# Kernel optimization log

Hardware: AMD Instinct MI355X
Metric: run time of the kernel (lower is better)

The kernel has to match this reference:

```python
import jax, jax.numpy as jnp
import numpy as np

B, S, D, E, F = 2, 2048, 1024, 8, 4096


def setup_inputs() -> dict:
    key = jax.random.key(0)
    k1, k2, k3, k4 = jax.random.split(key, 4)
    x = jax.random.normal(k1, (B, S, D), dtype=jnp.float32)
    gate_w = jax.random.normal(k2, (E, D), dtype=jnp.float32) * 0.02
    w1 = jax.random.normal(k3, (E, D, F), dtype=jnp.float32) * 0.02
    w2 = jax.random.normal(k4, (E, F, D), dtype=jnp.float32) * 0.02
    return {"x": x, "gate_w": gate_w, "w1": w1, "w2": w2}


def reference(x, gate_w, w1, w2):
    b, s, d = x.shape
    n_experts = w1.shape[0]
    tokens = x.reshape(-1, d)                      # (T, D)
    logits = tokens @ gate_w.T                     # (T, E) router (Linear, no bias)
    expert_ids = jnp.argmax(logits, axis=-1)       # top-1 routing (T,)
    dispatch = jax.nn.one_hot(expert_ids, n_experts, dtype=tokens.dtype)  # (T, E)
    # dense all-experts reference of the grouped GEMM: h_e = tokens @ w1[e]
    h = jnp.einsum('td,edf->etf', tokens, w1)      # (E, T, F)
    h = jax.nn.gelu(h, approximate=False)          # torch F.gelu default = exact erf
    out_e = jnp.einsum('etf,efd->etd', h, w2)      # (E, T, D)
    # scatter back: each token takes exactly its assigned expert's output
    out = jnp.einsum('etd,te->td', out_e, dispatch)
    return out.reshape(b, s, d)
```

## Files before the change

kernel.cpp:

```cpp
#include <hip/hip_runtime.h>
#include <hip/hip_bf16.h>
#include <math.h>

#define T_TOK 4096
#define D_DIM 1024
#define E_EXP 8
#define F_DIM 4096
#define BM 128
#define BN 128
#define BK 32
#define LDK 40
#define MAX_TILES 40
#define KSPLIT 4

typedef __attribute__((ext_vector_type(8))) short short8;
typedef __attribute__((ext_vector_type(4))) short short4v;
typedef __attribute__((ext_vector_type(4))) float float4v;

__device__ __forceinline__ short f2b(float f) {
    union { float f; unsigned u; } v; v.f = f;
    unsigned r = v.u + 0x7fffu + ((v.u >> 16) & 1u);
    return (short)(r >> 16);
}

typedef const __attribute__((address_space(1))) unsigned gu32;
typedef __attribute__((address_space(3))) unsigned lu32;
__device__ __forceinline__ void gload16(const void* g, void* l) {
    __builtin_amdgcn_global_load_lds((gu32*)g, (lu32*)l, 16, 0, 0);
}

__global__ void router_kernel(const float* __restrict__ x, const float* __restrict__ gw,
                              int* __restrict__ eid, int* __restrict__ rnk,
                              int* __restrict__ counts) {
    int lane = threadIdx.x & 63;
    int wave = threadIdx.x >> 6;
    int t = blockIdx.x * 4 + wave;
    const float* xr = x + (size_t)t * D_DIM;
    float p[E_EXP];
#pragma unroll
    for (int e = 0; e < E_EXP; ++e) p[e] = 0.f;
#pragma unroll
    for (int i = 0; i < D_DIM / 64; ++i) {
        float v = xr[lane + 64 * i];
#pragma unroll
        for (int e = 0; e < E_EXP; ++e)
            p[e] = fmaf(v, gw[e * D_DIM + lane + 64 * i], p[e]);
    }
#pragma unroll
    for (int off = 32; off > 0; off >>= 1) {
#pragma unroll
        for (int e = 0; e < E_EXP; ++e) p[e] += __shfl_down(p[e], off, 64);
    }
    if (lane == 0) {
        int best = 0; float bv = p[0];
#pragma unroll
        for (int e = 1; e < E_EXP; ++e) if (p[e] > bv) { bv = p[e]; best = e; }
        eid[t] = best;
        rnk[t] = atomicAdd(&counts[best], 1);
    }
}

__global__ void prefix_kernel(const int* __restrict__ counts, int* __restrict__ offsets,
                              int* __restrict__ tmap) {
    int off = 0;
    offsets[0] = 0;
    int nt = 0;
    for (int e = 0; e < E_EXP; ++e) {
        int c = counts[e];
        for (int m0 = 0; m0 < c; m0 += BM) {
            tmap[nt * 3 + 0] = e;
            tmap[nt * 3 + 1] = off + m0;
            tmap[nt * 3 + 2] = (c - m0 < BM) ? (c - m0) : BM;
            ++nt;
        }
        off += c;
        offsets[e + 1] = off;
    }
    for (; nt < MAX_TILES; ++nt) tmap[nt * 3 + 2] = 0;
}

__global__ void scatter_kernel(const int* __restrict__ eid, const int* __restrict__ rnk,
                               const int* __restrict__ offsets, int* __restrict__ sorted) {
    int t = blockIdx.x * 256 + threadIdx.x;
    sorted[offsets[eid[t]] + rnk[t]] = t;
}

__global__ __launch_bounds__(256) void xcvt_kernel(const float* __restrict__ src,
                                                   short* __restrict__ dst) {
    size_t i = ((size_t)blockIdx.x * 256 + threadIdx.x) * 4;
    float4v v = *(const float4v*)(src + i);
    short4v w;
#pragma unroll
    for (int q = 0; q < 4; ++q) w[q] = f2b(v[q]);
    *(short4v*)(dst + i) = w;
}

__global__ __launch_bounds__(256) void transpose_cvt(const float* __restrict__ src,
                                                     short* __restrict__ dst,
                                                     int R, int C) {
    __shared__ float t[64][65];
    size_t eoff = (size_t)blockIdx.z * R * C;
    const float* s = src + eoff;
    short* d = dst + eoff;
    int c0 = blockIdx.x * 64, r0 = blockIdx.y * 64;
    int tr = threadIdx.x >> 4;
    int tc = (threadIdx.x & 15) * 4;
#pragma unroll
    for (int p = 0; p < 4; ++p) {
        int r = tr + p * 16;
        float4v v = *(const float4v*)(s + (size_t)(r0 + r) * C + (c0 + tc));
        t[r][tc + 0] = v[0]; t[r][tc + 1] = v[1]; t[r][tc + 2] = v[2]; t[r][tc + 3] = v[3];
    }
    __syncthreads();
#pragma unroll
    for (int p = 0; p < 4; ++p) {
        int cl = tr + p * 16;
        short4v w;
#pragma unroll
        for (int q = 0; q < 4; ++q) w[q] = f2b(t[tc + q][cl]);
        *(short4v*)(d + (size_t)(c0 + cl) * R + (r0 + tc)) = w;
    }
}


__global__ __launch_bounds__(256) void gemm1_kernel(const short* __restrict__ xb,
                                                    const short* __restrict__ w1t,
                                                    const int* __restrict__ sorted,
                                                    const int* __restrict__ tmap,
                                                    short* __restrict__ hb) {
    __shared__ __align__(16) short As[4096];
    __shared__ __align__(16) short Bs[4096];
    __shared__ int srow[BM];
    int mt = blockIdx.y;
    int m_count = tmap[mt * 3 + 2];
    if (m_count == 0) return;
    int e = tmap[mt * 3 + 0];
    int row0 = tmap[mt * 3 + 1];
    int n0 = blockIdx.x * BN;
    int tid = threadIdx.x;
    if (tid < BM) srow[tid] = sorted[row0 + (tid < m_count ? tid : m_count - 1)];
    __syncthreads();

    int lane = tid & 63, wave = tid >> 6;
    int wm = (wave & 1) * 64, wn = (wave >> 1) * 64;
    int s0 = 2 * wave, s1 = s0 + 1;
    int c0s = s0 >> 1, m0s = (s0 & 1) * 64 + lane;
    int c1s = s1 >> 1, m1s = (s1 & 1) * 64 + lane;
    const short* aptr0 = xb + (size_t)srow[m0s] * D_DIM + c0s * 8;
    const short* aptr1 = xb + (size_t)srow[m1s] * D_DIM + c1s * 8;
    const short* wbase = w1t + (size_t)e * F_DIM * D_DIM;
    const short* bptr0 = wbase + (size_t)(n0 + m0s) * D_DIM + c0s * 8;
    const short* bptr1 = wbase + (size_t)(n0 + m1s) * D_DIM + c1s * 8;
    short* al0 = &As[s0 * 512];
    short* al1 = &As[s1 * 512];
    short* bl0 = &Bs[s0 * 512];
    short* bl1 = &Bs[s1 * 512];

    float4v acc[4][4];
#pragma unroll
    for (int i = 0; i < 4; ++i)
#pragma unroll
        for (int j = 0; j < 4; ++j) acc[i][j] = (float4v)(0.f);

    int cr = (lane >> 4) * 128;
    int lm = lane & 15;
    for (int k0 = 0; k0 < D_DIM; k0 += BK) {
        gload16(aptr0 + k0, al0);
        gload16(aptr1 + k0, al1);
        gload16(bptr0 + k0, bl0);
        gload16(bptr1 + k0, bl1);
        __syncthreads();
        short8 af[4], bf[4];
#pragma unroll
        for (int i = 0; i < 4; ++i)
            af[i] = *(const short8*)&As[(cr + wm + i * 16 + lm) * 8];
#pragma unroll
        for (int j = 0; j < 4; ++j)
            bf[j] = *(const short8*)&Bs[(cr + wn + j * 16 + lm) * 8];
#pragma unroll
        for (int i = 0; i < 4; ++i)
#pragma unroll
            for (int j = 0; j < 4; ++j)
                acc[i][j] = __builtin_amdgcn_mfma_f32_16x16x32_bf16(af[i], bf[j], acc[i][j], 0, 0, 0);
        __syncthreads();
    }
    int rbase = (lane >> 4) * 4;
    int cbase = lane & 15;
#pragma unroll
    for (int i = 0; i < 4; ++i) {
#pragma unroll
        for (int r = 0; r < 4; ++r) {
            int row = wm + i * 16 + rbase + r;
            if (row < m_count) {
                short* hp = hb + (size_t)(row0 + row) * F_DIM + n0 + wn + cbase;
#pragma unroll
                for (int j = 0; j < 4; ++j) {
                    float s = acc[i][j][r];
                    float g = 0.5f * s * (1.f + erff(s * 0.70710678118f));
                    hp[j * 16] = f2b(g);
                }
            }
        }
    }
}

__global__ __launch_bounds__(256) void gemm2_kernel(const short* __restrict__ hb,
                                                    const short* __restrict__ w2t,
                                                    const int* __restrict__ tmap,
                                                    float* __restrict__ pbuf) {
    __shared__ __align__(16) short As[4096];
    __shared__ __align__(16) short Bs[4096];
    int mt = blockIdx.y;
    int m_count = tmap[mt * 3 + 2];
    if (m_count == 0) return;
    int e = tmap[mt * 3 + 0];
    int row0 = tmap[mt * 3 + 1];
    int n0 = blockIdx.x * BN;
    int kp = blockIdx.z;
    int kbase = kp * (F_DIM / KSPLIT);
    int tid = threadIdx.x;
    int lane = tid & 63, wave = tid >> 6;
    int wm = (wave & 1) * 64, wn = (wave >> 1) * 64;
    int s0 = 2 * wave, s1 = s0 + 1;
    int c0s = s0 >> 1, m0s = (s0 & 1) * 64 + lane;
    int c1s = s1 >> 1, m1s = (s1 & 1) * 64 + lane;
    int am0 = m0s < m_count ? m0s : m_count - 1;
    int am1 = m1s < m_count ? m1s : m_count - 1;
    const short* aptr0 = hb + (size_t)(row0 + am0) * F_DIM + kbase + c0s * 8;
    const short* aptr1 = hb + (size_t)(row0 + am1) * F_DIM + kbase + c1s * 8;
    const short* wbase = w2t + (size_t)e * D_DIM * F_DIM;
    const short* bptr0 = wbase + (size_t)(n0 + m0s) * F_DIM + kbase + c0s * 8;
    const short* bptr1 = wbase + (size_t)(n0 + m1s) * F_DIM + kbase + c1s * 8;
    short* al0 = &As[s0 * 512];
    short* al1 = &As[s1 * 512];
    short* bl0 = &Bs[s0 * 512];
    short* bl1 = &Bs[s1 * 512];

    float4v acc[4][4];
#pragma unroll
    for (int i = 0; i < 4; ++i)
#pragma unroll
        for (int j = 0; j < 4; ++j) acc[i][j] = (float4v)(0.f);

    int cr = (lane >> 4) * 128;
    int lm = lane & 15;
    for (int k0 = 0; k0 < F_DIM / KSPLIT; k0 += BK) {
        gload16(aptr0 + k0, al0);
        gload16(aptr1 + k0, al1);
        gload16(bptr0 + k0, bl0);
        gload16(bptr1 + k0, bl1);
        __syncthreads();
        short8 af[4], bf[4];
#pragma unroll
        for (int i = 0; i < 4; ++i)
            af[i] = *(const short8*)&As[(cr + wm + i * 16 + lm) * 8];
#pragma unroll
        for (int j = 0; j < 4; ++j)
            bf[j] = *(const short8*)&Bs[(cr + wn + j * 16 + lm) * 8];
#pragma unroll
        for (int i = 0; i < 4; ++i)
#pragma unroll
            for (int j = 0; j < 4; ++j)
                acc[i][j] = __builtin_amdgcn_mfma_f32_16x16x32_bf16(af[i], bf[j], acc[i][j], 0, 0, 0);
        __syncthreads();
    }
    float* pb = pbuf + (size_t)kp * T_TOK * D_DIM;
    int rbase = (lane >> 4) * 4;
    int cbase = lane & 15;
#pragma unroll
    for (int i = 0; i < 4; ++i) {
#pragma unroll
        for (int r = 0; r < 4; ++r) {
            int row = wm + i * 16 + rbase + r;
            if (row < m_count) {
                float* pp = pb + (size_t)(row0 + row) * D_DIM + n0 + wn + cbase;
#pragma unroll
                for (int j = 0; j < 4; ++j) pp[j * 16] = acc[i][j][r];
            }
        }
    }
}

__global__ __launch_bounds__(256) void reduce_kernel(const float* __restrict__ pbuf,
                                                     const int* __restrict__ sorted,
                                                     float* __restrict__ out) {
    int s = blockIdx.x;
    int d = threadIdx.x * 4;
    const float* p = pbuf + (size_t)s * D_DIM + d;
    float4v a = *(const float4v*)(p);
    a += *(const float4v*)(p + (size_t)1 * T_TOK * D_DIM);
    a += *(const float4v*)(p + (size_t)2 * T_TOK * D_DIM);
    a += *(const float4v*)(p + (size_t)3 * T_TOK * D_DIM);
    *(float4v*)(out + (size_t)sorted[s] * D_DIM + d) = a;
}

__global__ __launch_bounds__(256) void gemm1_fb(const float* __restrict__ x,
                                                const float* __restrict__ w1,
                                                const int* __restrict__ sorted,
                                                const int* __restrict__ tmap,
                                                short* __restrict__ hbuf) {
    __shared__ short As[BM * LDK];
    __shared__ short Bs[BN * LDK];
    __shared__ int srow[BM];
    int mt = blockIdx.y;
    int m_count = tmap[mt * 3 + 2];
    if (m_count == 0) return;
    int e = tmap[mt * 3 + 0];
    int row0 = tmap[mt * 3 + 1];
    int n0 = blockIdx.x * BN;
    int tid = threadIdx.x;
    if (tid < BM) srow[tid] = sorted[row0 + (tid < m_count ? tid : m_count - 1)];
    __syncthreads();
    int lane = tid & 63, wave = tid >> 6;
    int wm = (wave & 1) * 64, wn = (wave >> 1) * 64;
    float4v acc[4][4];
#pragma unroll
    for (int i = 0; i < 4; ++i)
#pragma unroll
        for (int j = 0; j < 4; ++j) acc[i][j] = (float4v)(0.f);
    int ar = tid >> 1, ac = (tid & 1) * 16, bn = tid & 127, bq = (tid >> 7) * 16;
    const float* abase = x + (size_t)srow[ar] * D_DIM + ac;
    const float* bbase = w1 + (size_t)e * D_DIM * F_DIM + (size_t)bq * F_DIM + (n0 + bn);
    for (int k0 = 0; k0 < D_DIM; k0 += BK) {
        {
            const float* ap = abase + k0;
            float4v f0 = *(const float4v*)(ap);
            float4v f1 = *(const float4v*)(ap + 4);
            float4v f2 = *(const float4v*)(ap + 8);
            float4v f3 = *(const float4v*)(ap + 12);
            short8 t0, t1;
#pragma unroll
            for (int c = 0; c < 4; ++c) {
                t0[c] = f2b(f0[c]); t0[4 + c] = f2b(f1[c]);
                t1[c] = f2b(f2[c]); t1[4 + c] = f2b(f3[c]);
            }
            *(short8*)(&As[ar * LDK + ac]) = t0;
            *(short8*)(&As[ar * LDK + ac + 8]) = t1;
        }
        {
            const float* bp = bbase + (size_t)k0 * F_DIM;
            float v[16];
#pragma unroll
            for (int j = 0; j < 16; ++j) v[j] = bp[(size_t)j * F_DIM];
            short8 t0, t1;
#pragma unroll
            for (int j = 0; j < 8; ++j) { t0[j] = f2b(v[j]); t1[j] = f2b(v[8 + j]); }
            *(short8*)(&Bs[bn * LDK + bq]) = t0;
            *(short8*)(&Bs[bn * LDK + bq + 8]) = t1;
        }
        __syncthreads();
        short8 af[4], bf[4];
#pragma unroll
        for (int i = 0; i < 4; ++i)
            af[i] = *(const short8*)(&As[(wm + i * 16 + (lane & 15)) * LDK + (lane >> 4) * 8]);
#pragma unroll
        for (int j = 0; j < 4; ++j)
            bf[j] = *(const short8*)(&Bs[(wn + j * 16 + (lane & 15)) * LDK + (lane >> 4) * 8]);
#pragma unroll
        for (int i = 0; i < 4; ++i)
#pragma unroll
            for (int j = 0; j < 4; ++j)
                acc[i][j] = __builtin_amdgcn_mfma_f32_16x16x32_bf16(af[i], bf[j], acc[i][j], 0, 0, 0);
        __syncthreads();
    }
    int rbase = (lane >> 4) * 4, cbase = lane & 15;
#pragma unroll
    for (int i = 0; i < 4; ++i) {
#pragma unroll
        for (int r = 0; r < 4; ++r) {
            int row = wm + i * 16 + rbase + r;
            if (row < m_count) {
                short* hp = hbuf + (size_t)(row0 + row) * F_DIM + n0 + wn + cbase;
#pragma unroll
                for (int j = 0; j < 4; ++j) {
                    float s = acc[i][j][r];
                    float g = 0.5f * s * (1.f + erff(s * 0.70710678118f));
                    hp[j * 16] = f2b(g);
                }
            }
        }
    }
}

__global__ __launch_bounds__(256) void gemm2_fb(const short* __restrict__ hbuf,
                                                const float* __restrict__ w2,
                                                const int* __restrict__ sorted,
                                                const int* __restrict__ tmap,
                                                float* __restrict__ out) {
    __shared__ short As[BM * LDK];
    __shared__ short Bs[BN * LDK];
    __shared__ int srow[BM];
    int mt = blockIdx.y;
    int m_count = tmap[mt * 3 + 2];
    if (m_count == 0) return;
    int e = tmap[mt * 3 + 0];
    int row0 = tmap[mt * 3 + 1];
    int n0 = blockIdx.x * BN;
    int tid = threadIdx.x;
    if (tid < BM) srow[tid] = sorted[row0 + (tid < m_count ? tid : m_count - 1)];
    __syncthreads();
    int lane = tid & 63, wave = tid >> 6;
    int wm = (wave & 1) * 64, wn = (wave >> 1) * 64;
    float4v acc[4][4];
#pragma unroll
    for (int i = 0; i < 4; ++i)
#pragma unroll
        for (int j = 0; j < 4; ++j) acc[i][j] = (float4v)(0.f);
    int ar = tid >> 1, ac = (tid & 1) * 16, bn = tid & 127, bq = (tid >> 7) * 16;
    int arc = ar < m_count ? ar : m_count - 1;
    const short* abase = hbuf + (size_t)(row0 + arc) * F_DIM + ac;
    const float* bbase = w2 + (size_t)e * F_DIM * D_DIM + (size_t)bq * D_DIM + (n0 + bn);
    for (int k0 = 0; k0 < F_DIM; k0 += BK) {
        {
            const short* ap = abase + k0;
            *(short8*)(&As[ar * LDK + ac]) = *(const short8*)(ap);
            *(short8*)(&As[ar * LDK + ac + 8]) = *(const short8*)(ap + 8);
        }
        {
            const float* bp = bbase + (size_t)k0 * D_DIM;
            float v[16];
#pragma unroll
            for (int j = 0; j < 16; ++j) v[j] = bp[(size_t)j * D_DIM];
            short8 t0, t1;
#pragma unroll
            for (int j = 0; j < 8; ++j) { t0[j] = f2b(v[j]); t1[j] = f2b(v[8 + j]); }
            *(short8*)(&Bs[bn * LDK + bq]) = t0;
            *(short8*)(&Bs[bn * LDK + bq + 8]) = t1;
        }
        __syncthreads();
        short8 af[4], bf[4];
#pragma unroll
        for (int i = 0; i < 4; ++i)
            af[i] = *(const short8*)(&As[(wm + i * 16 + (lane & 15)) * LDK + (lane >> 4) * 8]);
#pragma unroll
        for (int j = 0; j < 4; ++j)
            bf[j] = *(const short8*)(&Bs[(wn + j * 16 + (lane & 15)) * LDK + (lane >> 4) * 8]);
#pragma unroll
        for (int i = 0; i < 4; ++i)
#pragma unroll
            for (int j = 0; j < 4; ++j)
                acc[i][j] = __builtin_amdgcn_mfma_f32_16x16x32_bf16(af[i], bf[j], acc[i][j], 0, 0, 0);
        __syncthreads();
    }
    int rbase = (lane >> 4) * 4, cbase = lane & 15;
#pragma unroll
    for (int i = 0; i < 4; ++i) {
#pragma unroll
        for (int r = 0; r < 4; ++r) {
            int row = wm + i * 16 + rbase + r;
            if (row < m_count) {
                float* op = out + (size_t)srow[row] * D_DIM + n0 + wn + cbase;
#pragma unroll
                for (int j = 0; j < 4; ++j) op[j * 16] = acc[i][j][r];
            }
        }
    }
}

extern "C" void kernel_launch(void* const* d_in, const int* in_sizes, int n_in,
                              void* d_out, int out_size, void* d_ws, size_t ws_size,
                              hipStream_t stream) {
    const float* x  = (const float*)d_in[0];
    const float* gw = (const float*)d_in[1];
    const float* w1 = (const float*)d_in[2];
    const float* w2 = (const float*)d_in[3];
    float* out = (float*)d_out;
    char* ws = (char*)d_ws;

    int* counts  = (int*)(ws);
    int* offsets = (int*)(ws + 64);
    int* tmap    = (int*)(ws + 128);
    int* eid     = (int*)(ws + 1024);
    int* rnk     = (int*)(ws + 17408);
    int* sorted  = (int*)(ws + 33792);

    const size_t XB_OFF  = 65536;
    const size_t W1T_OFF = XB_OFF  + (size_t)T_TOK * D_DIM * 2;
    const size_t W2T_OFF = W1T_OFF + (size_t)E_EXP * D_DIM * F_DIM * 2;
    const size_t HB_OFF  = W2T_OFF + (size_t)E_EXP * D_DIM * F_DIM * 2;
    const size_t PB_OFF  = HB_OFF  + (size_t)T_TOK * F_DIM * 2;
    const size_t NEED    = PB_OFF  + (size_t)KSPLIT * T_TOK * D_DIM * 4;

    hipMemsetAsync(counts, 0, 32, stream);
    router_kernel<<<T_TOK / 4, 256, 0, stream>>>(x, gw, eid, rnk, counts);
    prefix_kernel<<<1, 1, 0, stream>>>(counts, offsets, tmap);
    scatter_kernel<<<T_TOK / 256, 256, 0, stream>>>(eid, rnk, offsets, sorted);

    if (ws_size >= NEED) {
        short* xb   = (short*)(ws + XB_OFF);
        short* w1t  = (short*)(ws + W1T_OFF);
        short* w2t  = (short*)(ws + W2T_OFF);
        short* hb   = (short*)(ws + HB_OFF);
        float* pbuf = (float*)(ws + PB_OFF);
        xcvt_kernel<<<(T_TOK * D_DIM) / 1024, 256, 0, stream>>>(x, xb);
        transpose_cvt<<<dim3(F_DIM / 64, D_DIM / 64, E_EXP), 256, 0, stream>>>(w1, w1t, D_DIM, F_DIM);
        transpose_cvt<<<dim3(D_DIM / 64, F_DIM / 64, E_EXP), 256, 0, stream>>>(w2, w2t, F_DIM, D_DIM);
        gemm1_kernel<<<dim3(F_DIM / BN, MAX_TILES), 256, 0, stream>>>(xb, w1t, sorted, tmap, hb);
        gemm2_kernel<<<dim3(D_DIM / BN, MAX_TILES, KSPLIT), 256, 0, stream>>>(hb, w2t, tmap, pbuf);
        reduce_kernel<<<T_TOK, 256, 0, stream>>>(pbuf, sorted, out);
    } else {
        short* hbuf = (short*)(ws + 51200);
        gemm1_fb<<<dim3(F_DIM / BN, MAX_TILES), 256, 0, stream>>>(x, w1, sorted, tmap, hbuf);
        gemm2_fb<<<dim3(D_DIM / BN, MAX_TILES), 256, 0, stream>>>(hbuf, w2, sorted, tmap, out);
    }
}
```

Before: 600.9 us.

## Double-buffer LDS tiles in both expert GEMMs and widen transpose stores

Both grouped GEMM kernels now keep two LDS buffers for the A and B tiles. The next K-slice is issued with gload16 right after the barrier, while MFMAs run on the current buffer, and one of the two barriers per iteration is removed. The weight transpose-convert kernel now writes two 16-byte short8 vectors per thread instead of four 8-byte stores. Doubling LDS per block may reduce occupancy. The single-barrier scheme depends on gload16's completion semantics being correct with only one sync per step.

```diff
diff --git a/kernel.cpp b/kernel.cpp
--- a/kernel.cpp
+++ b/kernel.cpp
@@ -112,14 +112,14 @@
         t[r][tc + 0] = v[0]; t[r][tc + 1] = v[1]; t[r][tc + 2] = v[2]; t[r][tc + 3] = v[3];
     }
     __syncthreads();
-#pragma unroll
-    for (int p = 0; p < 4; ++p) {
-        int cl = tr + p * 16;
-        short4v w;
-#pragma unroll
-        for (int q = 0; q < 4; ++q) w[q] = f2b(t[tc + q][cl]);
-        *(short4v*)(d + (size_t)(c0 + cl) * R + (r0 + tc)) = w;
-    }
+    int nl = threadIdx.x >> 2;
+    int kl = (threadIdx.x & 3) * 16;
+    short8 w0, w1;
+#pragma unroll
+    for (int q = 0; q < 8; ++q) { w0[q] = f2b(t[kl + q][nl]); w1[q] = f2b(t[kl + 8 + q][nl]); }
+    short* dp = d + (size_t)(c0 + nl) * R + (r0 + kl);
+    *(short8*)(dp) = w0;
+    *(short8*)(dp + 8) = w1;
 }
 
 
@@ -128,8 +128,8 @@
                                                     const int* __restrict__ sorted,
                                                     const int* __restrict__ tmap,
                                                     short* __restrict__ hb) {
-    __shared__ __align__(16) short As[4096];
-    __shared__ __align__(16) short Bs[4096];
+    __shared__ __align__(16) short As[2][4096];
+    __shared__ __align__(16) short Bs[2][4096];
     __shared__ int srow[BM];
     int mt = blockIdx.y;
     int m_count = tmap[mt * 3 + 2];
@@ -151,10 +151,10 @@
     const short* wbase = w1t + (size_t)e * F_DIM * D_DIM;
     const short* bptr0 = wbase + (size_t)(n0 + m0s) * D_DIM + c0s * 8;
     const short* bptr1 = wbase + (size_t)(n0 + m1s) * D_DIM + c1s * 8;
-    short* al0 = &As[s0 * 512];
-    short* al1 = &As[s1 * 512];
-    short* bl0 = &Bs[s0 * 512];
-    short* bl1 = &Bs[s1 * 512];
+    short* al0[2] = { &As[0][s0 * 512], &As[1][s0 * 512] };
+    short* al1[2] = { &As[0][s1 * 512], &As[1][s1 * 512] };
+    short* bl0[2] = { &Bs[0][s0 * 512], &Bs[1][s0 * 512] };
+    short* bl1[2] = { &Bs[0][s1 * 512], &Bs[1][s1 * 512] };
 
     float4v acc[4][4];
 #pragma unroll
@@ -164,25 +164,30 @@
 
     int cr = (lane >> 4) * 128;
     int lm = lane & 15;
+    gload16(aptr0, al0[0]); gload16(aptr1, al1[0]);
+    gload16(bptr0, bl0[0]); gload16(bptr1, bl1[0]);
+    int cur = 0;
     for (int k0 = 0; k0 < D_DIM; k0 += BK) {
-        gload16(aptr0 + k0, al0);
-        gload16(aptr1 + k0, al1);
-        gload16(bptr0 + k0, bl0);
-        gload16(bptr1 + k0, bl1);
         __syncthreads();
+        int nk = k0 + BK;
+        if (nk < D_DIM) {
+            int nb = cur ^ 1;
+            gload16(aptr0 + nk, al0[nb]); gload16(aptr1 + nk, al1[nb]);
+            gload16(bptr0 + nk, bl0[nb]); gload16(bptr1 + nk, bl1[nb]);
+        }
         short8 af[4], bf[4];
 #pragma unroll
         for (int i = 0; i < 4; ++i)
-            af[i] = *(const short8*)&As[(cr + wm + i * 16 + lm) * 8];
+            af[i] = *(const short8*)&As[cur][(cr + wm + i * 16 + lm) * 8];
 #pragma unroll
         for (int j = 0; j < 4; ++j)
-            bf[j] = *(const short8*)&Bs[(cr + wn + j * 16 + lm) * 8];
+            bf[j] = *(const short8*)&Bs[cur][(cr + wn + j * 16 + lm) * 8];
 #pragma unroll
         for (int i = 0; i < 4; ++i)
 #pragma unroll
             for (int j = 0; j < 4; ++j)
                 acc[i][j] = __builtin_amdgcn_mfma_f32_16x16x32_bf16(af[i], bf[j], acc[i][j], 0, 0, 0);
-        __syncthreads();
+        cur ^= 1;
     }
     int rbase = (lane >> 4) * 4;
     int cbase = lane & 15;
@@ -208,8 +213,8 @@
                                                     const short* __restrict__ w2t,
                                                     const int* __restrict__ tmap,
                                                     float* __restrict__ pbuf) {
-    __shared__ __align__(16) short As[4096];
-    __shared__ __align__(16) short Bs[4096];
+    __shared__ __align__(16) short As[2][4096];
+    __shared__ __align__(16) short Bs[2][4096];
     int mt = blockIdx.y;
     int m_count = tmap[mt * 3 + 2];
     if (m_count == 0) return;
@@ -231,10 +236,10 @@
     const short* wbase = w2t + (size_t)e * D_DIM * F_DIM;
     const short* bptr0 = wbase + (size_t)(n0 + m0s) * F_DIM + kbase + c0s * 8;
     const short* bptr1 = wbase + (size_t)(n0 + m1s) * F_DIM + kbase + c1s * 8;
-    short* al0 = &As[s0 * 512];
-    short* al1 = &As[s1 * 512];
-    short* bl0 = &Bs[s0 * 512];
-    short* bl1 = &Bs[s1 * 512];
+    short* al0[2] = { &As[0][s0 * 512], &As[1][s0 * 512] };
+    short* al1[2] = { &As[0][s1 * 512], &As[1][s1 * 512] };
+    short* bl0[2] = { &Bs[0][s0 * 512], &Bs[1][s0 * 512] };
+    short* bl1[2] = { &Bs[0][s1 * 512], &Bs[1][s1 * 512] };
 
     float4v acc[4][4];
 #pragma unroll
@@ -244,25 +249,31 @@
 
     int cr = (lane >> 4) * 128;
     int lm = lane & 15;
-    for (int k0 = 0; k0 < F_DIM / KSPLIT; k0 += BK) {
-        gload16(aptr0 + k0, al0);
-        gload16(aptr1 + k0, al1);
-        gload16(bptr0 + k0, bl0);
-        gload16(bptr1 + k0, bl1);
+    gload16(aptr0, al0[0]); gload16(aptr1, al1[0]);
+    gload16(bptr0, bl0[0]); gload16(bptr1, bl1[0]);
+    int cur = 0;
+    const int KLEN = F_DIM / KSPLIT;
+    for (int k0 = 0; k0 < KLEN; k0 += BK) {
         __syncthreads();
+        int nk = k0 + BK;
+        if (nk < KLEN) {
+            int nb = cur ^ 1;
+            gload16(aptr0 + nk, al0[nb]); gload16(aptr1 + nk, al1[nb]);
+            gload16(bptr0 + nk, bl0[nb]); gload16(bptr1 + nk, bl1[nb]);
+        }
         short8 af[4], bf[4];
 #pragma unroll
         for (int i = 0; i < 4; ++i)
-            af[i] = *(const short8*)&As[(cr + wm + i * 16 + lm) * 8];
+            af[i] = *(const short8*)&As[cur][(cr + wm + i * 16 + lm) * 8];
 #pragma unroll
         for (int j = 0; j < 4; ++j)
-            bf[j] = *(const short8*)&Bs[(cr + wn + j * 16 + lm) * 8];
+            bf[j] = *(const short8*)&Bs[cur][(cr + wn + j * 16 + lm) * 8];
 #pragma unroll
         for (int i = 0; i < 4; ++i)
 #pragma unroll
             for (int j = 0; j < 4; ++j)
                 acc[i][j] = __builtin_amdgcn_mfma_f32_16x16x32_bf16(af[i], bf[j], acc[i][j], 0, 0, 0);
-        __syncthreads();
+        cur ^= 1;
     }
     float* pb = pbuf + (size_t)kp * T_TOK * D_DIM;
     int rbase = (lane >> 4) * 4;
```

New measurement: 608.9 us. No clear change (+1.3%).
